# Kernel optimization log

Measured on AMD Instinct MI355X. Metric: run time of the kernel, lower is better.

Reference implementation:

```python
import jax, jax.numpy as jnp
import numpy as np

COMMITMENT_COST = 0.25
NUM_EMBEDDINGS = 4096
EMBEDDING_DIM = 256


def setup_inputs() -> dict:
    key = jax.random.key(0)
    kx, ke = jax.random.split(key)
    x = jax.random.normal(kx, (64, 1024, EMBEDDING_DIM), dtype=jnp.float32)
    # nn.Embedding weight initialized uniform(-1/K, 1/K)
    emb = jax.random.uniform(ke, (NUM_EMBEDDINGS, EMBEDDING_DIM), dtype=jnp.float32,
                             minval=-1.0 / NUM_EMBEDDINGS, maxval=1.0 / NUM_EMBEDDINGS)
    return {"x": x, "emb": emb}


def reference(x, emb):
    D = emb.shape[1]
    flat_x = x.reshape(-1, D)                                    # [N, D]
    distances = (jnp.sum(flat_x * flat_x, axis=1, keepdims=True)
                 - 2.0 * flat_x @ emb.T
                 + jnp.sum(emb * emb, axis=1))
    indices = jnp.argmin(distances, axis=1)                      # [N]
    quantized = emb[indices].reshape(x.shape)                    # [..., D]
    e_latent_loss = jnp.mean((jax.lax.stop_gradient(quantized) - x) ** 2)
    q_latent_loss = jnp.mean((quantized - jax.lax.stop_gradient(x)) ** 2)
    loss = q_latent_loss + COMMITMENT_COST * e_latent_loss
    # straight-through estimator
    quantized = x + jax.lax.stop_gradient(quantized - x)
    return quantized, loss, indices[:, None]
```

## Files before the change

kernel.cpp:

```cpp
#include <hip/hip_runtime.h>
#include <math.h>

#define DIMD 256
#define KCODES 4096
#define NROWS 65536
#define QN (NROWS * DIMD)

constexpr int P1_BM = 64;
constexpr int P1_BN = 128;
constexpr int NT    = KCODES / P1_BN;
constexpr float TAU2 = 7.5e-4f;
constexpr float TAU2B = TAU2 + 1e-5f;
constexpr int CAP   = 48;
constexpr int NS    = 8;

typedef __attribute__((ext_vector_type(8))) short bf16x8;
typedef __attribute__((ext_vector_type(4))) float f32x4;

#define VM8() asm volatile("s_waitcnt vmcnt(8)" ::: "memory")
#define VM4() asm volatile("s_waitcnt vmcnt(4)" ::: "memory")
#define VM0() asm volatile("s_waitcnt vmcnt(0)" ::: "memory")

__device__ __forceinline__ unsigned short f2bf(float f) {
    unsigned int u = __builtin_bit_cast(unsigned int, f);
    u += 0x7fffu + ((u >> 16) & 1u);
    return (unsigned short)(u >> 16);
}

__device__ __forceinline__ float opaque(float v) {
    asm volatile("" : "+v"(v));
    return v;
}

__device__ __forceinline__ void gload_lds16(const void* g, void* l) {
    __builtin_amdgcn_global_load_lds(
        (const __attribute__((address_space(1))) unsigned int*)g,
        (__attribute__((address_space(3))) unsigned int*)l, 16, 0, 0);
}

__global__ void sx_kernel(const float* __restrict__ x, float* __restrict__ sx) {
    const int j   = threadIdx.x & 7;
    const int row = blockIdx.x * 32 + (threadIdx.x >> 3);
    const float* p = x + (size_t)row * DIMD;
    float total = 0.0f;
    #pragma unroll
    for (int half = 0; half < 2; ++half) {
        const float* b = p + half * 128;
        const float v0 = b[j];
        float r = opaque(v0 * v0);
        #pragma unroll
        for (int i = 8; i < 128; i += 8) {
            const float v = b[i + j];
            r += opaque(v * v);
        }
        const float s1  = r  + __shfl_xor(r, 1, 64);
        const float s2  = s1 + __shfl_xor(s1, 2, 64);
        const float res = s2 + __shfl_xor(s2, 4, 64);
        total = (half == 0) ? res : (total + res);
    }
    if (j == 0) sx[row] = total;
}

__global__ void se_kernel(const float* __restrict__ emb, float* __restrict__ se) {
    const int j   = threadIdx.x & 7;
    const int row = blockIdx.x * 32 + (threadIdx.x >> 3);
    const float* p = emb + (size_t)row * DIMD;
    float total = 0.0f;
    #pragma unroll
    for (int half = 0; half < 2; ++half) {
        const float* b = p + half * 128;
        const float v0 = b[j];
        float r = opaque(v0 * v0);
        #pragma unroll
        for (int i = 8; i < 128; i += 8) {
            const float v = b[i + j];
            r += opaque(v * v);
        }
        const float s1  = r  + __shfl_xor(r, 1, 64);
        const float s2  = s1 + __shfl_xor(s1, 2, 64);
        const float res = s2 + __shfl_xor(s2, 4, 64);
        total = (half == 0) ? res : (total + res);
    }
    if (j == 0) se[row] = total;
}

__global__ void conv_emb_kernel(const float* __restrict__ emb, unsigned short* __restrict__ embh) {
    const int i = blockIdx.x * blockDim.x + threadIdx.x;
    const float4 v = ((const float4*)emb)[i];
    ushort4 h;
    h.x = f2bf(v.x); h.y = f2bf(v.y); h.z = f2bf(v.z); h.w = f2bf(v.w);
    ((ushort4*)embh)[i] = h;
}

__global__ __launch_bounds__(256, 2)
void pass1_kernel(const float* __restrict__ x, const unsigned short* __restrict__ embh,
                  unsigned int* __restrict__ cand, int* __restrict__ cnt_out) {
    __shared__ unsigned short Bs[3][8192];
    __shared__ float part[4][32];
    __shared__ float tilemax[P1_BM];
    __shared__ int   cnts[P1_BM];

    const int t    = threadIdx.x;
    const int w    = t >> 6;
    const int lane = t & 63;
    const int quad = lane >> 4;
    const int lm   = lane & 15;
    const int wr   = w >> 1;
    const int wc   = w & 1;
    const int row0 = blockIdx.x * P1_BM;

    if (t < P1_BM) cnts[t] = 0;

    bf16x8 afr[2][8];
    #pragma unroll
    for (int f = 0; f < 2; ++f) {
        const float* xr = x + (size_t)(row0 + wr * 32 + f * 16 + lm) * DIMD + quad * 8;
        #pragma unroll
        for (int c = 0; c < 8; ++c) {
            const float4 v0 = *(const float4*)(xr + c * 32);
            const float4 v1 = *(const float4*)(xr + c * 32 + 4);
            bf16x8 h;
            h[0] = (short)f2bf(v0.x); h[1] = (short)f2bf(v0.y);
            h[2] = (short)f2bf(v0.z); h[3] = (short)f2bf(v0.w);
            h[4] = (short)f2bf(v1.x); h[5] = (short)f2bf(v1.y);
            h[6] = (short)f2bf(v1.z); h[7] = (short)f2bf(v1.w);
            afr[f][c] = h;
        }
    }

    auto stage = [&](int buf, int m) {
        const int c0  = (m >> 2) * P1_BN;
        const int kcb = (m & 3) * 64;
        #pragma unroll
        for (int i = 0; i < 4; ++i) {
            const int seg  = i * 4 + w;
            const int code = seg * 8 + (lane >> 3);
            const int kk   = ((lane & 7) ^ ((lane >> 3) & 7)) * 8;
            const unsigned short* src = embh + (size_t)(c0 + code) * DIMD + kcb + kk;
            gload_lds16(src, &Bs[buf][seg * 512]);
        }
    };

    stage(0, 0);
    stage(1, 1);
    int bc = 0;

    float rmg[2][4];
    #pragma unroll
    for (int f = 0; f < 2; ++f)
        #pragma unroll
        for (int reg = 0; reg < 4; ++reg) rmg[f][reg] = -INFINITY;

    for (int tile = 0; tile < NT; ++tile) {
        const int c0 = tile * P1_BN;
        f32x4 acc[2][4];
        #pragma unroll
        for (int f = 0; f < 2; ++f)
            #pragma unroll
            for (int g = 0; g < 4; ++g) acc[f][g] = (f32x4){0.f, 0.f, 0.f, 0.f};

        #pragma unroll
        for (int kb = 0; kb < 4; ++kb) {
            const int m = tile * 4 + kb;
            __syncthreads();
            int st = bc + 2; if (st >= 3) st -= 3;
            if (tile < NT - 1) {
                stage(st, m + 2);
                VM8();
            } else {
                if (kb == 0) { stage(st, m + 2); VM8(); }
                else if (kb == 1) { stage(st, m + 2); VM8(); }
                else if (kb == 2) { VM4(); }
                else { VM0(); }
            }
            __syncthreads();

            #pragma unroll
            for (int ks = 0; ks < 2; ++ks) {
                bf16x8 b[4];
                #pragma unroll
                for (int g = 0; g < 4; ++g) {
                    const int j = wc * 64 + g * 16 + lm;
                    b[g] = *(const bf16x8*)
                        &Bs[bc][j * 64 + ((((ks << 2) + quad) ^ (lm & 7)) << 3)];
                }
                #pragma unroll
                for (int f = 0; f < 2; ++f)
                    #pragma unroll
                    for (int g = 0; g < 4; ++g)
                        acc[f][g] = __builtin_amdgcn_mfma_f32_16x16x32_bf16(
                            afr[f][kb * 2 + ks], b[g], acc[f][g], 0, 0, 0);
            }

            if (kb == 3) {
                #pragma unroll
                for (int f = 0; f < 2; ++f) {
                    f32x4 mm4;
                    #pragma unroll
                    for (int reg = 0; reg < 4; ++reg) {
                        float mm = fmaxf(fmaxf(acc[f][0][reg], acc[f][1][reg]),
                                         fmaxf(acc[f][2][reg], acc[f][3][reg]));
                        #pragma unroll
                        for (int off = 1; off < 16; off <<= 1)
                            mm = fmaxf(mm, __shfl_xor(mm, off, 64));
                        mm4[reg] = mm;
                    }
                    if (lm == 0)
                        *(f32x4*)&part[w][f * 16 + quad * 4] = mm4;
                }
            }
            bc = (bc == 2) ? 0 : bc + 1;
        }

        __syncthreads();
        if (t < P1_BM) {
            const int trh = t >> 5, loc = t & 31;
            tilemax[t] = fmaxf(part[trh * 2][loc], part[trh * 2 + 1][loc]);
        }
        __syncthreads();

        #pragma unroll
        for (int f = 0; f < 2; ++f) {
            const f32x4 tm = *(const f32x4*)&tilemax[wr * 32 + f * 16 + quad * 4];
            #pragma unroll
            for (int reg = 0; reg < 4; ++reg) {
                rmg[f][reg] = fmaxf(rmg[f][reg], tm[reg]);
                const float thr = rmg[f][reg] - TAU2;
                const int r = wr * 32 + f * 16 + quad * 4 + reg;
                #pragma unroll
                for (int g = 0; g < 4; ++g) {
                    const float dv = acc[f][g][reg];
                    if (dv > thr) {
                        const int slot = atomicAdd(&cnts[r], 1);
                        if (slot < CAP) {
                            const unsigned int ub =
                                __builtin_bit_cast(unsigned int, fmaxf(dv, 0.0f));
                            cand[(size_t)(row0 + r) * CAP + slot] =
                                (ub & 0xFFFFF000u) |
                                (unsigned int)(c0 + wc * 64 + g * 16 + lm);
                        }
                    }
                }
            }
        }
        VM0();
    }
    __syncthreads();
    if (t < P1_BM) cnt_out[row0 + t] = (cnts[t] > CAP) ? -1 : cnts[t];
}

__global__ __launch_bounds__(256, 4)
void pass2_kernel(const float* __restrict__ x, const float* __restrict__ emb,
                  const float* __restrict__ sx, const float* __restrict__ se,
                  const unsigned int* __restrict__ cand, const int* __restrict__ cnt,
                  float* __restrict__ out, float* __restrict__ partial) {
    __shared__ float4 xsh[4][64];
    __shared__ float4 esh[4][NS][64];
    const int w = threadIdx.x >> 6, lane = threadIdx.x & 63;
    const int row = blockIdx.x * 4 + w;
    const int n = cnt[row];
    const float sxr = sx[row];
    const float4* emb4 = (const float4*)emb;

    const float4 myx = ((const float4*)(x + (size_t)row * DIMD))[lane];
    xsh[w][lane] = myx;
    const float4* xs4 = &xsh[w][0];

    float bestd = INFINITY;
    int   bestc = 0x7fffffff;
    int   wslot = 0x7fffffff;

    if (n >= 1 && n <= CAP) {
        float dtil = -INFINITY;
        int   code = 0;
        if (lane < n) {
            const unsigned int word = cand[(size_t)row * CAP + lane];
            dtil = __builtin_bit_cast(float, word & 0xFFFFF000u);
            code = (int)(word & 0xFFFu);
        }
        float mx = dtil;
        #pragma unroll
        for (int off = 1; off < 64; off <<= 1)
            mx = fmaxf(mx, __shfl_xor(mx, off, 64));
        const bool active = (lane < n) && (dtil > mx - TAU2B);
        const unsigned long long mask = __ballot(active);
        const int nact = __popcll(mask);
        const int slot = __popcll(mask & ((1ull << lane) - 1ull));
        unsigned long long mm = mask;
        const int ns = nact < NS ? nact : NS;
        for (int i = 0; i < ns; ++i) {
            const int li = __ffsll(mm) - 1;
            mm &= mm - 1;
            const int bc = __shfl(code, li, 64);
            gload_lds16(emb4 + (size_t)bc * 64 + lane, &esh[w][i][0]);
        }
        VM0();
        if (active) {
            float a = 0.0f;
            if (slot < NS) {
                const float4* ep4 = &esh[w][slot][0];
                #pragma unroll
                for (int d4 = 0; d4 < DIMD / 4; ++d4) {
                    const float4 ev = ep4[d4];
                    const float4 xv = xs4[d4];
                    a = fmaf(xv.x, ev.x, a);
                    a = fmaf(xv.y, ev.y, a);
                    a = fmaf(xv.z, ev.z, a);
                    a = fmaf(xv.w, ev.w, a);
                }
            } else {
                const float4* ep4 = emb4 + (size_t)code * 64;
                #pragma unroll
                for (int d4 = 0; d4 < DIMD / 4; ++d4) {
                    const float4 ev = ep4[d4];
                    const float4 xv = xs4[d4];
                    a = fmaf(xv.x, ev.x, a);
                    a = fmaf(xv.y, ev.y, a);
                    a = fmaf(xv.z, ev.z, a);
                    a = fmaf(xv.w, ev.w, a);
                }
            }
            const float t1 = sxr - 2.0f * a;
            bestd = t1 + se[code];
            bestc = code;
            wslot = slot;
        }
    } else {
        for (int c = lane; c < KCODES; c += 64) {
            const float* ep = emb + (size_t)c * DIMD;
            float a = 0.0f;
            for (int d4 = 0; d4 < DIMD / 4; ++d4) {
                const float4 xv = xs4[d4];
                const float4 ev = ((const float4*)ep)[d4];
                a = fmaf(xv.x, ev.x, a);
                a = fmaf(xv.y, ev.y, a);
                a = fmaf(xv.z, ev.z, a);
                a = fmaf(xv.w, ev.w, a);
            }
            const float t1 = sxr - 2.0f * a;
            const float dd = t1 + se[c];
            if (dd < bestd || (dd == bestd && c < bestc)) { bestd = dd; bestc = c; }
        }
    }
    #pragma unroll
    for (int off = 32; off > 0; off >>= 1) {
        const float od = __shfl_down(bestd, off, 64);
        const int   oc = __shfl_down(bestc, off, 64);
        const int   os = __shfl_down(wslot, off, 64);
        if (od < bestd || (od == bestd && oc < bestc)) {
            bestd = od; bestc = oc; wslot = os;
        }
    }
    bestc = __shfl(bestc, 0, 64);
    wslot = __shfl(wslot, 0, 64);

    const float4 e4 = (wslot < NS) ? esh[w][wslot][lane]
                                   : emb4[(size_t)bestc * 64 + lane];
    ((float4*)(out + (size_t)row * DIMD))[lane] = e4;
    const float dx = e4.x - myx.x, dy = e4.y - myx.y,
                dz = e4.z - myx.z, dw = e4.w - myx.w;
    float s = dx * dx + dy * dy + dz * dz + dw * dw;
    #pragma unroll
    for (int off = 32; off > 0; off >>= 1) s += __shfl_down(s, off, 64);
    if (lane == 0) {
        partial[row] = s;
        out[QN + 1 + row] = (float)bestc;
    }
}

__global__ void loss_reduce_kernel(const float* __restrict__ partial, float* __restrict__ out) {
    const int t = threadIdx.x;
    double s = 0.0;
    for (int i = t; i < NROWS; i += 256) s += (double)partial[i];
    __shared__ double tsum[256];
    tsum[t] = s;
    __syncthreads();
    #pragma unroll
    for (int off = 128; off > 0; off >>= 1) {
        if (t < off) tsum[t] += tsum[t + off];
        __syncthreads();
    }
    if (t == 0) out[QN] = (float)(tsum[0] * (1.25 / (double)QN));
}

extern "C" void kernel_launch(void* const* d_in, const int* in_sizes, int n_in,
                              void* d_out, int out_size, void* d_ws, size_t ws_size,
                              hipStream_t stream) {
    const float* x   = (const float*)d_in[0];
    const float* emb = (const float*)d_in[1];
    float* out = (float*)d_out;

    char* ws = (char*)d_ws;
    unsigned short* embh = (unsigned short*)ws;           ws += (size_t)KCODES * DIMD * 2;
    float* sx  = (float*)ws;                              ws += (size_t)NROWS * 4;
    float* se  = (float*)ws;                              ws += (size_t)KCODES * 4;
    unsigned int* cand = (unsigned int*)ws;               ws += (size_t)NROWS * CAP * 4;
    int*   cnt  = (int*)ws;                               ws += (size_t)NROWS * 4;
    float* partial = (float*)ws;

    conv_emb_kernel<<<KCODES * DIMD / 4 / 256, 256, 0, stream>>>(emb, embh);
    sx_kernel<<<NROWS / 32, 256, 0, stream>>>(x, sx);
    se_kernel<<<KCODES / 32, 256, 0, stream>>>(emb, se);
    pass1_kernel<<<NROWS / P1_BM, 256, 0, stream>>>(x, embh, cand, cnt);
    pass2_kernel<<<NROWS / 4, 256, 0, stream>>>(x, emb, sx, se, cand, cnt, out, partial);
    loss_reduce_kernel<<<1, 256, 0, stream>>>(partial, out);
}
```

Measured before the change: 782.4 us.

## Double-buffer wider K chunks in pass1 and stage candidates in LDS

Pass1 now stages the bf16 codebook through two LDS buffers of 128-wide K chunks instead of three 64-wide ones. This halves the barrier and wait rounds per code tile and lets the per-tile max reduction run once after the K loop. Candidate words are collected in a shared-memory array and written to global memory in one coalesced copy at the end, which removes scattered global stores and the per-tile vmcnt(0) drain. Pass2 issues its candidate load unconditionally and early, alongside the x load. That load reads past the row's 48 slots for lanes 48-63, and past the end of the buffer on the last row, and it raises pass1's LDS footprint.

```diff
diff --git a/kernel.cpp b/kernel.cpp
--- a/kernel.cpp
+++ b/kernel.cpp
@@ -9,6 +9,7 @@
 constexpr int P1_BM = 64;
 constexpr int P1_BN = 128;
 constexpr int NT    = KCODES / P1_BN;
+constexpr int NCHUNK = NT * 2;
 constexpr float TAU2 = 7.5e-4f;
 constexpr float TAU2B = TAU2 + 1e-5f;
 constexpr int CAP   = 48;
@@ -18,7 +19,6 @@
 typedef __attribute__((ext_vector_type(4))) float f32x4;
 
 #define VM8() asm volatile("s_waitcnt vmcnt(8)" ::: "memory")
-#define VM4() asm volatile("s_waitcnt vmcnt(4)" ::: "memory")
 #define VM0() asm volatile("s_waitcnt vmcnt(0)" ::: "memory")
 
 __device__ __forceinline__ unsigned short f2bf(float f) {
@@ -95,7 +95,8 @@
 __global__ __launch_bounds__(256, 2)
 void pass1_kernel(const float* __restrict__ x, const unsigned short* __restrict__ embh,
                   unsigned int* __restrict__ cand, int* __restrict__ cnt_out) {
-    __shared__ unsigned short Bs[3][8192];
+    __shared__ unsigned short Bs[2][16384];
+    __shared__ unsigned int cand_lds[P1_BM * CAP];
     __shared__ float part[4][32];
     __shared__ float tilemax[P1_BM];
     __shared__ int   cnts[P1_BM];
@@ -129,21 +130,20 @@
     }
 
     auto stage = [&](int buf, int m) {
-        const int c0  = (m >> 2) * P1_BN;
-        const int kcb = (m & 3) * 64;
-        #pragma unroll
-        for (int i = 0; i < 4; ++i) {
-            const int seg  = i * 4 + w;
-            const int code = seg * 8 + (lane >> 3);
-            const int kk   = ((lane & 7) ^ ((lane >> 3) & 7)) * 8;
-            const unsigned short* src = embh + (size_t)(c0 + code) * DIMD + kcb + kk;
+        const int c0  = (m >> 1) * P1_BN;
+        const int kcb = (m & 1) * 128;
+        #pragma unroll
+        for (int i = 0; i < 8; ++i) {
+            const int seg = i * 4 + w;
+            const int c   = seg * 4 + (lane >> 4);
+            const int kk  = ((lane & 15) ^ (c & 15)) * 8;
+            const unsigned short* src = embh + (size_t)(c0 + c) * DIMD + kcb + kk;
             gload_lds16(src, &Bs[buf][seg * 512]);
         }
     };
 
     stage(0, 0);
-    stage(1, 1);
-    int bc = 0;
+    int buf = 0;
 
     float rmg[2][4];
     #pragma unroll
@@ -160,62 +160,56 @@
             for (int g = 0; g < 4; ++g) acc[f][g] = (f32x4){0.f, 0.f, 0.f, 0.f};
 
         #pragma unroll
-        for (int kb = 0; kb < 4; ++kb) {
-            const int m = tile * 4 + kb;
+        for (int kb = 0; kb < 2; ++kb) {
+            const int m = tile * 2 + kb;
             __syncthreads();
-            int st = bc + 2; if (st >= 3) st -= 3;
-            if (tile < NT - 1) {
-                stage(st, m + 2);
+            if (m + 1 < NCHUNK) {
+                stage(buf ^ 1, m + 1);
                 VM8();
             } else {
-                if (kb == 0) { stage(st, m + 2); VM8(); }
-                else if (kb == 1) { stage(st, m + 2); VM8(); }
-                else if (kb == 2) { VM4(); }
-                else { VM0(); }
+                VM0();
             }
             __syncthreads();
 
             #pragma unroll
-            for (int ks = 0; ks < 2; ++ks) {
+            for (int ks = 0; ks < 4; ++ks) {
                 bf16x8 b[4];
                 #pragma unroll
                 for (int g = 0; g < 4; ++g) {
-                    const int j = wc * 64 + g * 16 + lm;
+                    const int c = wc * 64 + g * 16 + lm;
                     b[g] = *(const bf16x8*)
-                        &Bs[bc][j * 64 + ((((ks << 2) + quad) ^ (lm & 7)) << 3)];
+                        &Bs[buf][c * 128 + ((((ks << 2) + quad) ^ lm) << 3)];
                 }
                 #pragma unroll
                 for (int f = 0; f < 2; ++f)
                     #pragma unroll
                     for (int g = 0; g < 4; ++g)
                         acc[f][g] = __builtin_amdgcn_mfma_f32_16x16x32_bf16(
-                            afr[f][kb * 2 + ks], b[g], acc[f][g], 0, 0, 0);
-            }
-
-            if (kb == 3) {
-                #pragma unroll
-                for (int f = 0; f < 2; ++f) {
-                    f32x4 mm4;
-                    #pragma unroll
-                    for (int reg = 0; reg < 4; ++reg) {
-                        float mm = fmaxf(fmaxf(acc[f][0][reg], acc[f][1][reg]),
-                                         fmaxf(acc[f][2][reg], acc[f][3][reg]));
-                        #pragma unroll
-                        for (int off = 1; off < 16; off <<= 1)
-                            mm = fmaxf(mm, __shfl_xor(mm, off, 64));
-                        mm4[reg] = mm;
-                    }
-                    if (lm == 0)
-                        *(f32x4*)&part[w][f * 16 + quad * 4] = mm4;
-                }
-            }
-            bc = (bc == 2) ? 0 : bc + 1;
+                            afr[f][kb * 4 + ks], b[g], acc[f][g], 0, 0, 0);
+            }
+            buf ^= 1;
+        }
+
+        #pragma unroll
+        for (int f = 0; f < 2; ++f) {
+            f32x4 mm4;
+            #pragma unroll
+            for (int reg = 0; reg < 4; ++reg) {
+                float mm = fmaxf(fmaxf(acc[f][0][reg], acc[f][1][reg]),
+                                 fmaxf(acc[f][2][reg], acc[f][3][reg]));
+                #pragma unroll
+                for (int off = 1; off < 16; off <<= 1)
+                    mm = fmaxf(mm, __shfl_xor(mm, off, 64));
+                mm4[reg] = mm;
+            }
+            if (lm == 0)
+                *(f32x4*)&part[w][f * 16 + quad * 4] = mm4;
         }
 
         __syncthreads();
         if (t < P1_BM) {
-            const int trh = t >> 5, loc = t & 31;
-            tilemax[t] = fmaxf(part[trh * 2][loc], part[trh * 2 + 1][loc]);
+            const int trg = t >> 5, loc = t & 31;
+            tilemax[t] = fmaxf(part[trg * 2][loc], part[trg * 2 + 1][loc]);
         }
         __syncthreads();
 
@@ -235,7 +229,7 @@
                         if (slot < CAP) {
                             const unsigned int ub =
                                 __builtin_bit_cast(unsigned int, fmaxf(dv, 0.0f));
-                            cand[(size_t)(row0 + r) * CAP + slot] =
+                            cand_lds[r * CAP + slot] =
                                 (ub & 0xFFFFF000u) |
                                 (unsigned int)(c0 + wc * 64 + g * 16 + lm);
                         }
@@ -243,9 +237,16 @@
                 }
             }
         }
-        VM0();
     }
     __syncthreads();
+
+    {
+        const uint4* src = (const uint4*)cand_lds;
+        uint4* dst = (uint4*)(cand + (size_t)row0 * CAP);
+        #pragma unroll
+        for (int i = 0; i < P1_BM * CAP / 4 / 256; ++i)
+            dst[i * 256 + t] = src[i * 256 + t];
+    }
     if (t < P1_BM) cnt_out[row0 + t] = (cnts[t] > CAP) ? -1 : cnts[t];
 }
 
@@ -259,10 +260,11 @@
     const int w = threadIdx.x >> 6, lane = threadIdx.x & 63;
     const int row = blockIdx.x * 4 + w;
     const int n = cnt[row];
+    const unsigned int word = cand[(size_t)row * CAP + lane];
     const float sxr = sx[row];
+    const float4 myx = ((const float4*)(x + (size_t)row * DIMD))[lane];
     const float4* emb4 = (const float4*)emb;
 
-    const float4 myx = ((const float4*)(x + (size_t)row * DIMD))[lane];
     xsh[w][lane] = myx;
     const float4* xs4 = &xsh[w][0];
 
@@ -271,13 +273,9 @@
     int   wslot = 0x7fffffff;
 
     if (n >= 1 && n <= CAP) {
-        float dtil = -INFINITY;
-        int   code = 0;
-        if (lane < n) {
-            const unsigned int word = cand[(size_t)row * CAP + lane];
-            dtil = __builtin_bit_cast(float, word & 0xFFFFF000u);
-            code = (int)(word & 0xFFFu);
-        }
+        const float dtil = (lane < n)
+            ? __builtin_bit_cast(float, word & 0xFFFFF000u) : -INFINITY;
+        const int code = (int)(word & 0xFFFu);
         float mx = dtil;
         #pragma unroll
         for (int off = 1; off < 64; off <<= 1)
```

Result: faster. 744.0 us (-4.9%).
